# Performance work log

Measured on AMD Instinct MI355X. Metric: run time of the kernel, lower is better.

The kernel has to match this reference:

```python
import jax, jax.numpy as jnp
import numpy as np

S, H, R, Z, P = 268, 1024, 8, 8, 4
A = S - Z - P          # actual_hidden_dim = 256
E = min(Z, P)          # min_embed_dim = 4
B = 8192


def setup_inputs() -> dict:
    key = jax.random.key(0)
    ks = jax.random.split(key, 16)
    def g(k, shape, scale=0.02):
        return jax.random.normal(k, shape, dtype=jnp.float32) * scale
    return dict(
        t=jax.random.uniform(ks[0], (1,), dtype=jnp.float32) * 24.0,
        state=jax.random.normal(ks[1], (B, S), dtype=jnp.float32),
        W0=g(ks[2], (H, S + 2)), b0=jnp.zeros((H,), jnp.float32),
        res_W1=g(ks[3], (R, H, H)), res_b1=jnp.zeros((R, H), jnp.float32),
        res_W2=g(ks[4], (R, H, H)), res_b2=jnp.zeros((R, H), jnp.float32),
        Wf=g(ks[5], (S, H)), bf=jnp.zeros((S,), jnp.float32),
        lp_in_w=g(ks[6], (3 * E, E)), lp_in_b=jnp.zeros((3 * E,), jnp.float32),
        lp_out_w=g(ks[7], (E, E)), lp_out_b=jnp.zeros((E,), jnp.float32),
        ta_in_w=g(ks[8], (3 * A, A)), ta_in_b=jnp.zeros((3 * A,), jnp.float32),
        ta_out_w=g(ks[9], (A, A)), ta_out_b=jnp.zeros((A,), jnp.float32),
        loc_proj_w=g(ks[10], (E, Z)), loc_proj_b=jnp.zeros((E,), jnp.float32),
        loc_back_w=g(ks[11], (Z, E)), loc_back_b=jnp.zeros((Z,), jnp.float32),
    )


def reference(t, state, W0, b0, res_W1, res_b1, res_W2, res_b2, Wf, bf,
              lp_in_w, lp_in_b, lp_out_w, lp_out_b,
              ta_in_w, ta_in_b, ta_out_w, ta_out_b,
              loc_proj_w, loc_proj_b, loc_back_w, loc_back_b):
    Bn = state.shape[0]
    # time features: [sin(2*pi*t/24), cos(2*pi*t/24)] broadcast to [B, 2]
    ang = t * (2.0 * jnp.pi / 24.0)
    t_vec = jnp.broadcast_to(jnp.concatenate([jnp.sin(ang), jnp.cos(ang)]), (Bn, 2))

    # core MLP trunk: Linear -> ReLU -> R residual blocks -> Linear
    x = jnp.concatenate([state, t_vec], axis=-1)
    h = jax.nn.relu(x @ W0.T + b0)

    def block(h, p):
        W1, b1, W2, b2 = p
        return jnp.tanh(h + jnp.tanh(h @ W1.T + b1) @ W2.T + b2), None

    h, _ = jax.lax.scan(block, h, (res_W1, res_b1, res_W2, res_b2))
    core = h @ Wf.T + bf  # [B, S]

    # Attention deltas. Both MHA calls have key/value seq_len == 1, so the
    # softmax over a single key is exactly 1.0 and the output reduces exactly
    # to out_proj(v_proj(value)); Q/K projections (and the padded time query)
    # cancel mathematically. Same math as nn.MultiheadAttention here.
    h_part = state[:, :A]
    loc = state[:, A:A + Z]
    loc_p = loc @ loc_proj_w.T + loc_proj_b                   # [B, E]
    v = loc_p @ lp_in_w[2 * E:].T + lp_in_b[2 * E:]           # V projection
    enhanced_loc = v @ lp_out_w.T + lp_out_b                  # out projection
    delta_loc = (enhanced_loc - loc_p) @ loc_back_w.T + loc_back_b  # [B, Z]

    v2 = h_part @ ta_in_w[2 * A:].T + ta_in_b[2 * A:]
    enhanced_h = v2 @ ta_out_w.T + ta_out_b
    delta_h = enhanced_h - h_part                             # [B, A]

    delta = jnp.concatenate(
        [delta_h, delta_loc, jnp.zeros((Bn, P), state.dtype)], axis=-1)
    return core + 0.1 * delta
```

## Files before the change

### kernel.cpp

```cpp
#include <hip/hip_runtime.h>
#include <hip/hip_bf16.h>


typedef unsigned short u16;
typedef __bf16 bf16x8 __attribute__((ext_vector_type(8)));
typedef float f32x4 __attribute__((ext_vector_type(4)));

__device__ __forceinline__ u16 f2b(float f) {
  union { float f; unsigned u; } v; v.f = f;
  unsigned r = v.u + 0x7FFFu + ((v.u >> 16) & 1u);
  return (u16)(r >> 16);
}
__device__ __forceinline__ float b2f(u16 s) {
  union { unsigned u; float f; } v; v.u = ((unsigned)s) << 16;
  return v.f;
}

__device__ __forceinline__ void g2l16(const u16* g, u16* l) {
  __builtin_amdgcn_global_load_lds(
      (__attribute__((address_space(1))) void*)g,
      (__attribute__((address_space(3))) void*)l, 16, 0, 0);
}

template<int MODE, int KK, int LDA>
__global__ __launch_bounds__(256, 2)
void pgemm(const u16* __restrict__ A, const u16* __restrict__ W,
           const float* __restrict__ bias, const u16* __restrict__ resid,
           void* __restrict__ outp, int nreal, int ldo)
{
  __shared__ __align__(16) u16 As[2][128 * 64];
  __shared__ __align__(16) u16 Bs[2][128 * 64];
  const int tid  = threadIdx.x;
  const int wave = tid >> 6;
  const int lane = tid & 63;
  const int m0 = blockIdx.x << 7;
  const int n0 = blockIdx.y << 7;
  const int wr = wave >> 1, wc = wave & 1;
  const int lrow = lane & 15, quad = lane >> 4;
  const int sw = lrow & 7;

  const int srow  = lane >> 3;
  const int sperm = ((lane & 7) ^ (srow & 7)) << 3;

  const u16* Ag = A + (size_t)(m0 + wave * 32 + srow) * LDA + sperm;
  const u16* Bg = W + (size_t)(n0 + wave * 32 + srow) * KK + sperm;
  u16* AsW0 = &As[0][(wave * 32) * 64];
  u16* AsW1 = &As[1][(wave * 32) * 64];
  u16* BsW0 = &Bs[0][(wave * 32) * 64];
  u16* BsW1 = &Bs[1][(wave * 32) * 64];

  f32x4 acc[4][4];
#pragma unroll
  for (int i = 0; i < 4; i++)
#pragma unroll
    for (int j = 0; j < 4; j++) { f32x4 z = {0.f,0.f,0.f,0.f}; acc[i][j] = z; }

#pragma unroll
  for (int g = 0; g < 4; g++) {
    g2l16(Ag + (size_t)g * 8 * LDA, AsW0 + g * 8 * 64);
    g2l16(Bg + (size_t)g * 8 * KK,  BsW0 + g * 8 * 64);
  }
  __syncthreads();

  const int P = KK / 64;
  for (int p = 0; p < P; p++) {
    if (p + 1 < P) {
      const int ko = (p + 1) << 6;
      u16* aD = ((p + 1) & 1) ? AsW1 : AsW0;
      u16* bD = ((p + 1) & 1) ? BsW1 : BsW0;
#pragma unroll
      for (int g = 0; g < 4; g++) {
        g2l16(Ag + (size_t)g * 8 * LDA + ko, aD + g * 8 * 64);
        g2l16(Bg + (size_t)g * 8 * KK  + ko, bD + g * 8 * 64);
      }
    }
    const u16* aS = (p & 1) ? &As[1][0] : &As[0][0];
    const u16* bS = (p & 1) ? &Bs[1][0] : &Bs[0][0];
#pragma unroll
    for (int s = 0; s < 2; s++) {
      const int phys = (s * 4 + quad) ^ sw;
      bf16x8 af[4], bfr[4];
#pragma unroll
      for (int i = 0; i < 4; i++)
        af[i] = *(const bf16x8*)&aS[(wr * 64 + i * 16 + lrow) * 64 + phys * 8];
#pragma unroll
      for (int j = 0; j < 4; j++)
        bfr[j] = *(const bf16x8*)&bS[(wc * 64 + j * 16 + lrow) * 64 + phys * 8];
#pragma unroll
      for (int i = 0; i < 4; i++)
#pragma unroll
        for (int j = 0; j < 4; j++)
          acc[i][j] = __builtin_amdgcn_mfma_f32_16x16x32_bf16(af[i], bfr[j], acc[i][j], 0, 0, 0);
    }
    __syncthreads();
  }

  auto th = [](float x) {
    x = fminf(fmaxf(x, -40.f), 40.f);
    float a = __builtin_amdgcn_exp2f(2.88539008177793f * x);
    return (a - 1.f) * __builtin_amdgcn_rcpf(a + 1.f);
  };

#pragma unroll
  for (int i = 0; i < 4; i++) {
    const int rowb = m0 + wr * 64 + i * 16 + quad * 4;
#pragma unroll
    for (int j = 0; j < 4; j++) {
      const int col = n0 + wc * 64 + j * 16 + lrow;
      const float bi = (col < nreal) ? bias[col] : 0.f;
#pragma unroll
      for (int r = 0; r < 4; r++) {
        const int row = rowb + r;
        float v = acc[i][j][r] + bi;
        if (MODE == 0) {
          v = v > 0.f ? v : 0.f;
          ((u16*)outp)[(size_t)row * ldo + col] = f2b(v);
        } else if (MODE == 1) {
          ((u16*)outp)[(size_t)row * ldo + col] = f2b(th(v));
        } else if (MODE == 2) {
          v += b2f(resid[(size_t)row * ldo + col]);
          ((u16*)outp)[(size_t)row * ldo + col] = f2b(th(v));
        } else if (MODE == 3) {
          if (col < nreal) ((float*)outp)[(size_t)row * ldo + col] = v;
        }
      }
    }
  }
}

__global__ __launch_bounds__(256, 4)
void gemm_bt(const u16* __restrict__ A, const u16* __restrict__ B,
             const float* __restrict__ bias, u16* __restrict__ outp,
             int K, int lda, int ldo)
{
  __shared__ __align__(16) u16 As[64 * 64];
  __shared__ __align__(16) u16 Bs[128 * 64];
  const int tid  = threadIdx.x;
  const int wave = tid >> 6;
  const int lane = tid & 63;
  const int m0 = blockIdx.y << 6;
  const int n0 = blockIdx.x << 7;
  const int wr = wave >> 1, wc = wave & 1;
  const int lrow = lane & 15, quad = lane >> 4;
  const int srow  = lane >> 3;
  const int sperm = ((lane & 7) ^ (srow & 7)) << 3;

  const u16* Ag0 = A + (size_t)(m0 + wave * 16 +  0 + srow) * lda + sperm;
  const u16* Ag1 = A + (size_t)(m0 + wave * 16 +  8 + srow) * lda + sperm;
  const u16* Bg0 = B + (size_t)(n0 + wave * 32 +  0 + srow) * K + sperm;
  const u16* Bg1 = B + (size_t)(n0 + wave * 32 +  8 + srow) * K + sperm;
  const u16* Bg2 = B + (size_t)(n0 + wave * 32 + 16 + srow) * K + sperm;
  const u16* Bg3 = B + (size_t)(n0 + wave * 32 + 24 + srow) * K + sperm;
  u16* Al0 = &As[(wave * 16 +  0) * 64];
  u16* Al1 = &As[(wave * 16 +  8) * 64];
  u16* Bl0 = &Bs[(wave * 32 +  0) * 64];
  u16* Bl1 = &Bs[(wave * 32 +  8) * 64];
  u16* Bl2 = &Bs[(wave * 32 + 16) * 64];
  u16* Bl3 = &Bs[(wave * 32 + 24) * 64];

  f32x4 acc[2][4];
#pragma unroll
  for (int i = 0; i < 2; i++)
#pragma unroll
    for (int j = 0; j < 4; j++) { f32x4 z = {0.f,0.f,0.f,0.f}; acc[i][j] = z; }

  const int swz = lrow & 7;

  for (int k0 = 0; k0 < K; k0 += 64) {
    if (k0) __syncthreads();
    g2l16(Ag0 + k0, Al0);
    g2l16(Ag1 + k0, Al1);
    g2l16(Bg0 + k0, Bl0);
    g2l16(Bg1 + k0, Bl1);
    g2l16(Bg2 + k0, Bl2);
    g2l16(Bg3 + k0, Bl3);
    __syncthreads();
#pragma unroll
    for (int s = 0; s < 2; s++) {
      const int c = (s * 4 + quad) ^ swz;
      bf16x8 af[2], bfr[4];
#pragma unroll
      for (int i = 0; i < 2; i++)
        af[i] = *(const bf16x8*)&As[(wr * 32 + i * 16 + lrow) * 64 + c * 8];
#pragma unroll
      for (int j = 0; j < 4; j++)
        bfr[j] = *(const bf16x8*)&Bs[(wc * 64 + j * 16 + lrow) * 64 + c * 8];
#pragma unroll
      for (int i = 0; i < 2; i++)
#pragma unroll
        for (int j = 0; j < 4; j++)
          acc[i][j] = __builtin_amdgcn_mfma_f32_16x16x32_bf16(af[i], bfr[j], acc[i][j], 0, 0, 0);
    }
  }

#pragma unroll
  for (int i = 0; i < 2; i++) {
    const int rowb = m0 + wr * 32 + i * 16 + quad * 4;
#pragma unroll
    for (int j = 0; j < 4; j++) {
      const int col = n0 + wc * 64 + j * 16 + lrow;
      const float bi = bias[col];
#pragma unroll
      for (int r = 0; r < 4; r++)
        outp[(size_t)(rowb + r) * ldo + col] = f2b(acc[i][j][r] + bi);
    }
  }
}

__global__ void conv_bulk(const float* __restrict__ w1, const float* __restrict__ w2,
                          u16* __restrict__ o1, u16* __restrict__ o2)
{
  const int n4 = (8 * 1024 * 1024) / 4;
  int i = blockIdx.x * 256 + threadIdx.x;
  const float* src; u16* dst;
  if (i < n4) { src = w1; dst = o1; }
  else        { i -= n4; if (i >= n4) return; src = w2; dst = o2; }
  float4 v = ((const float4*)src)[i];
  unsigned p0 = (unsigned)f2b(v.x) | ((unsigned)f2b(v.y) << 16);
  unsigned p1 = (unsigned)f2b(v.z) | ((unsigned)f2b(v.w) << 16);
  uint2 pk; pk.x = p0; pk.y = p1;
  ((uint2*)dst)[i] = pk;
}

__global__ void conv_misc(const float* __restrict__ W0, const float* __restrict__ Wf,
                          const float* __restrict__ ta_in_w, const float* __restrict__ ta_out_w,
                          const float* __restrict__ state, const float* __restrict__ t,
                          u16* __restrict__ w0_bf, u16* __restrict__ wf_bf,
                          u16* __restrict__ taA, u16* __restrict__ taB,
                          u16* __restrict__ x_bf)
{
  int i = blockIdx.x * 256 + threadIdx.x;
  const int nW0 = 1024 * 384;
  const int nWf = 384 * 1024;
  const int nTa = 256 * 256;
  const int nX  = 8192 * 384;
  if (i < nW0) {
    int o = i / 384, k = i - o * 384;
    w0_bf[i] = (k < 270) ? f2b(W0[o * 270 + k]) : (u16)0;
    return;
  }
  i -= nW0;
  if (i < nWf) {
    int n = i >> 10;
    wf_bf[i] = (n < 268) ? f2b(Wf[i]) : (u16)0;
    return;
  }
  i -= nWf;
  if (i < nTa) { taA[i] = f2b(ta_in_w[512 * 256 + i]); return; }
  i -= nTa;
  if (i < nTa) { taB[i] = f2b(ta_out_w[i]); return; }
  i -= nTa;
  if (i < nX) {
    int r = i / 384, c = i - r * 384;
    u16 v;
    if (c < 268) v = f2b(state[r * 268 + c]);
    else if (c == 268) { float ang = t[0] * 0.2617993877991494f; v = f2b(sinf(ang)); }
    else if (c == 269) { float ang = t[0] * 0.2617993877991494f; v = f2b(cosf(ang)); }
    else v = 0;
    x_bf[i] = v;
  }
}

__global__ void add_delta(float* __restrict__ out, const u16* __restrict__ eh,
                          const float* __restrict__ state,
                          const float* __restrict__ lp_in_w, const float* __restrict__ lp_in_b,
                          const float* __restrict__ lp_out_w, const float* __restrict__ lp_out_b,
                          const float* __restrict__ loc_proj_w, const float* __restrict__ loc_proj_b,
                          const float* __restrict__ loc_back_w, const float* __restrict__ loc_back_b)
{
  const int idx = blockIdx.x * 256 + threadIdx.x;
  if (idx >= 8192 * 268) return;
  const int row = idx / 268;
  const int col = idx - row * 268;
  if (col < 256) {
    out[idx] += 0.1f * (b2f(eh[row * 256 + col]) - state[idx]);
  } else if (col < 264) {
    const float* srow = state + row * 268 + 256;
    float locp[4], vv[4], dd[4];
#pragma unroll
    for (int e = 0; e < 4; e++) {
      float s = loc_proj_b[e];
#pragma unroll
      for (int z = 0; z < 8; z++) s += loc_proj_w[e * 8 + z] * srow[z];
      locp[e] = s;
    }
#pragma unroll
    for (int e = 0; e < 4; e++) {
      float s = lp_in_b[8 + e];
#pragma unroll
      for (int j = 0; j < 4; j++) s += lp_in_w[(8 + e) * 4 + j] * locp[j];
      vv[e] = s;
    }
#pragma unroll
    for (int e = 0; e < 4; e++) {
      float s = lp_out_b[e];
#pragma unroll
      for (int j = 0; j < 4; j++) s += lp_out_w[e * 4 + j] * vv[j];
      dd[e] = s - locp[e];
    }
    const int z = col - 256;
    float s = loc_back_b[z];
#pragma unroll
    for (int e = 0; e < 4; e++) s += loc_back_w[z * 4 + e] * dd[e];
    out[idx] += 0.1f * s;
  }
}

extern "C" void kernel_launch(void* const* d_in, const int* in_sizes, int n_in,
                              void* d_out, int out_size, void* d_ws, size_t ws_size,
                              hipStream_t stream)
{
  const float* t          = (const float*)d_in[0];
  const float* state      = (const float*)d_in[1];
  const float* W0         = (const float*)d_in[2];
  const float* b0         = (const float*)d_in[3];
  const float* rW1        = (const float*)d_in[4];
  const float* rb1        = (const float*)d_in[5];
  const float* rW2        = (const float*)d_in[6];
  const float* rb2        = (const float*)d_in[7];
  const float* Wf         = (const float*)d_in[8];
  const float* bfv        = (const float*)d_in[9];
  const float* lp_in_w    = (const float*)d_in[10];
  const float* lp_in_b    = (const float*)d_in[11];
  const float* lp_out_w   = (const float*)d_in[12];
  const float* lp_out_b   = (const float*)d_in[13];
  const float* ta_in_w    = (const float*)d_in[14];
  const float* ta_in_b    = (const float*)d_in[15];
  const float* ta_out_w   = (const float*)d_in[16];
  const float* ta_out_b   = (const float*)d_in[17];
  const float* loc_proj_w = (const float*)d_in[18];
  const float* loc_proj_b = (const float*)d_in[19];
  const float* loc_back_w = (const float*)d_in[20];
  const float* loc_back_b = (const float*)d_in[21];
  float* out = (float*)d_out;

  char* ws = (char*)d_ws;
  auto alloc = [&](size_t bytes) { char* p = ws; ws += (bytes + 255) & ~(size_t)255; return p; };
  u16* rw1_bf = (u16*)alloc((size_t)8 * 1024 * 1024 * 2);
  u16* rw2_bf = (u16*)alloc((size_t)8 * 1024 * 1024 * 2);
  u16* w0_bf  = (u16*)alloc((size_t)1024 * 384 * 2);
  u16* wf_bf  = (u16*)alloc((size_t)384 * 1024 * 2);
  u16* taA_bf = (u16*)alloc((size_t)256 * 256 * 2);
  u16* taB_bf = (u16*)alloc((size_t)256 * 256 * 2);
  u16* x_bf   = (u16*)alloc((size_t)8192 * 384 * 2);
  u16* h_bf   = (u16*)alloc((size_t)8192 * 1024 * 2);
  u16* tmp_bf = (u16*)alloc((size_t)8192 * 1024 * 2);
  u16* v2_bf  = (u16*)alloc((size_t)8192 * 256 * 2);
  u16* eh_bf  = (u16*)alloc((size_t)8192 * 256 * 2);

  conv_bulk<<<16384, 256, 0, stream>>>(rW1, rW2, rw1_bf, rw2_bf);
  conv_misc<<<15872, 256, 0, stream>>>(W0, Wf, ta_in_w, ta_out_w, state, t,
                                       w0_bf, wf_bf, taA_bf, taB_bf, x_bf);

  pgemm<0, 384, 384><<<dim3(64, 8), 256, 0, stream>>>(x_bf, w0_bf, b0, nullptr, h_bf, 1024, 1024);

  for (int r = 0; r < 8; r++) {
    pgemm<1, 1024, 1024><<<dim3(64, 8), 256, 0, stream>>>(
        h_bf, rw1_bf + ((size_t)r << 20), rb1 + (r << 10), nullptr, tmp_bf, 1024, 1024);
    pgemm<2, 1024, 1024><<<dim3(64, 8), 256, 0, stream>>>(
        tmp_bf, rw2_bf + ((size_t)r << 20), rb2 + (r << 10), h_bf, h_bf, 1024, 1024);
  }

  gemm_bt<<<dim3(2, 128), 256, 0, stream>>>(x_bf, taA_bf, ta_in_b + 512, v2_bf, 256, 384, 256);
  gemm_bt<<<dim3(2, 128), 256, 0, stream>>>(v2_bf, taB_bf, ta_out_b, eh_bf, 256, 256, 256);

  pgemm<3, 1024, 1024><<<dim3(64, 3), 256, 0, stream>>>(h_bf, wf_bf, bfv, nullptr, out, 268, 268);

  add_delta<<<8576, 256, 0, stream>>>(out, eh_bf, state,
                                      lp_in_w, lp_in_b, lp_out_w, lp_out_b,
                                      loc_proj_w, loc_proj_b, loc_back_w, loc_back_b);
}
```

Measured before the change: 604.8 us.

## Enlarge GEMM block tile to 256x128 with 512 threads and dynamic LDS

Doubles the M extent of each pgemm block to 256 rows using 8 waves and moves the double-buffered A/B tiles into dynamic shared memory. Each weight tile is reused across twice as many rows, which halves global and LDS traffic for B per unit of output. In exchange each block needs about 96KB of LDS, which limits residency to one block per CU, and the grid shrinks to one block per CU, leaving less latency hiding.

```diff
diff --git a/kernel.cpp b/kernel.cpp
--- a/kernel.cpp
+++ b/kernel.cpp
@@ -23,17 +23,19 @@
 }
 
 template<int MODE, int KK, int LDA>
-__global__ __launch_bounds__(256, 2)
+__global__ __launch_bounds__(512, 2)
 void pgemm(const u16* __restrict__ A, const u16* __restrict__ W,
            const float* __restrict__ bias, const u16* __restrict__ resid,
            void* __restrict__ outp, int nreal, int ldo)
 {
-  __shared__ __align__(16) u16 As[2][128 * 64];
-  __shared__ __align__(16) u16 Bs[2][128 * 64];
+  extern __shared__ __align__(16) u16 sm[];
+  u16* Asb = sm;
+  u16* Bsb = sm + 2 * 256 * 64;
+
   const int tid  = threadIdx.x;
   const int wave = tid >> 6;
   const int lane = tid & 63;
-  const int m0 = blockIdx.x << 7;
+  const int m0 = blockIdx.x << 8;
   const int n0 = blockIdx.y << 7;
   const int wr = wave >> 1, wc = wave & 1;
   const int lrow = lane & 15, quad = lane >> 4;
@@ -43,11 +45,7 @@
   const int sperm = ((lane & 7) ^ (srow & 7)) << 3;
 
   const u16* Ag = A + (size_t)(m0 + wave * 32 + srow) * LDA + sperm;
-  const u16* Bg = W + (size_t)(n0 + wave * 32 + srow) * KK + sperm;
-  u16* AsW0 = &As[0][(wave * 32) * 64];
-  u16* AsW1 = &As[1][(wave * 32) * 64];
-  u16* BsW0 = &Bs[0][(wave * 32) * 64];
-  u16* BsW1 = &Bs[1][(wave * 32) * 64];
+  const u16* Bg = W + (size_t)(n0 + wave * 16 + srow) * KK + sperm;
 
   f32x4 acc[4][4];
 #pragma unroll
@@ -56,26 +54,29 @@
     for (int j = 0; j < 4; j++) { f32x4 z = {0.f,0.f,0.f,0.f}; acc[i][j] = z; }
 
 #pragma unroll
-  for (int g = 0; g < 4; g++) {
-    g2l16(Ag + (size_t)g * 8 * LDA, AsW0 + g * 8 * 64);
-    g2l16(Bg + (size_t)g * 8 * KK,  BsW0 + g * 8 * 64);
-  }
+  for (int g = 0; g < 4; g++)
+    g2l16(Ag + (size_t)g * 8 * LDA, Asb + (wave * 32 + g * 8) * 64);
+#pragma unroll
+  for (int g = 0; g < 2; g++)
+    g2l16(Bg + (size_t)g * 8 * KK, Bsb + (wave * 16 + g * 8) * 64);
   __syncthreads();
 
   const int P = KK / 64;
   for (int p = 0; p < P; p++) {
     if (p + 1 < P) {
       const int ko = (p + 1) << 6;
-      u16* aD = ((p + 1) & 1) ? AsW1 : AsW0;
-      u16* bD = ((p + 1) & 1) ? BsW1 : BsW0;
-#pragma unroll
-      for (int g = 0; g < 4; g++) {
-        g2l16(Ag + (size_t)g * 8 * LDA + ko, aD + g * 8 * 64);
-        g2l16(Bg + (size_t)g * 8 * KK  + ko, bD + g * 8 * 64);
-      }
-    }
-    const u16* aS = (p & 1) ? &As[1][0] : &As[0][0];
-    const u16* bS = (p & 1) ? &Bs[1][0] : &Bs[0][0];
+      const int bo = ((p + 1) & 1);
+      u16* aD = Asb + bo * 256 * 64;
+      u16* bD = Bsb + bo * 128 * 64;
+#pragma unroll
+      for (int g = 0; g < 4; g++)
+        g2l16(Ag + (size_t)g * 8 * LDA + ko, aD + (wave * 32 + g * 8) * 64);
+#pragma unroll
+      for (int g = 0; g < 2; g++)
+        g2l16(Bg + (size_t)g * 8 * KK + ko, bD + (wave * 16 + g * 8) * 64);
+    }
+    const u16* aS = Asb + (p & 1) * 256 * 64;
+    const u16* bS = Bsb + (p & 1) * 128 * 64;
 #pragma unroll
     for (int s = 0; s < 2; s++) {
       const int phys = (s * 4 + quad) ^ sw;
@@ -348,23 +349,33 @@
   u16* v2_bf  = (u16*)alloc((size_t)8192 * 256 * 2);
   u16* eh_bf  = (u16*)alloc((size_t)8192 * 256 * 2);
 
+  const int lds = (2 * 256 * 64 + 2 * 128 * 64) * 2;
+  hipFuncSetAttribute(reinterpret_cast<const void*>(pgemm<0, 384, 384>),
+                      hipFuncAttributeMaxDynamicSharedMemorySize, lds);
+  hipFuncSetAttribute(reinterpret_cast<const void*>(pgemm<1, 1024, 1024>),
+                      hipFuncAttributeMaxDynamicSharedMemorySize, lds);
+  hipFuncSetAttribute(reinterpret_cast<const void*>(pgemm<2, 1024, 1024>),
+                      hipFuncAttributeMaxDynamicSharedMemorySize, lds);
+  hipFuncSetAttribute(reinterpret_cast<const void*>(pgemm<3, 1024, 1024>),
+                      hipFuncAttributeMaxDynamicSharedMemorySize, lds);
+
   conv_bulk<<<16384, 256, 0, stream>>>(rW1, rW2, rw1_bf, rw2_bf);
   conv_misc<<<15872, 256, 0, stream>>>(W0, Wf, ta_in_w, ta_out_w, state, t,
                                        w0_bf, wf_bf, taA_bf, taB_bf, x_bf);
 
-  pgemm<0, 384, 384><<<dim3(64, 8), 256, 0, stream>>>(x_bf, w0_bf, b0, nullptr, h_bf, 1024, 1024);
+  pgemm<0, 384, 384><<<dim3(32, 8), 512, lds, stream>>>(x_bf, w0_bf, b0, nullptr, h_bf, 1024, 1024);
 
   for (int r = 0; r < 8; r++) {
-    pgemm<1, 1024, 1024><<<dim3(64, 8), 256, 0, stream>>>(
+    pgemm<1, 1024, 1024><<<dim3(32, 8), 512, lds, stream>>>(
         h_bf, rw1_bf + ((size_t)r << 20), rb1 + (r << 10), nullptr, tmp_bf, 1024, 1024);
-    pgemm<2, 1024, 1024><<<dim3(64, 8), 256, 0, stream>>>(
+    pgemm<2, 1024, 1024><<<dim3(32, 8), 512, lds, stream>>>(
         tmp_bf, rw2_bf + ((size_t)r << 20), rb2 + (r << 10), h_bf, h_bf, 1024, 1024);
   }
 
   gemm_bt<<<dim3(2, 128), 256, 0, stream>>>(x_bf, taA_bf, ta_in_b + 512, v2_bf, 256, 384, 256);
   gemm_bt<<<dim3(2, 128), 256, 0, stream>>>(v2_bf, taB_bf, ta_out_b, eh_bf, 256, 256, 256);
 
-  pgemm<3, 1024, 1024><<<dim3(64, 3), 256, 0, stream>>>(h_bf, wf_bf, bfv, nullptr, out, 268, 268);
+  pgemm<3, 1024, 1024><<<dim3(32, 3), 512, lds, stream>>>(h_bf, wf_bf, bfv, nullptr, out, 268, 268);
 
   add_delta<<<8576, 256, 0, stream>>>(out, eh_bf, state,
                                       lp_in_w, lp_in_b, lp_out_w, lp_out_b,
```

Result: faster. 579.6 us (-4.2%).
